# Optimization experiments

Hardware: AMD Instinct MI355X
Metric: run time of the kernel (lower is better)

The kernel has to match this reference:

```python
import jax, jax.numpy as jnp
import numpy as np

B, S, H = 1, 2048, 1024
NH, HD = 16, 64          # num heads, head dim (H = NH*HD)
NT = 1024                # param token num (qkv_slot_num = proj_slot_num)


def pattention(x, key_tokens, value_tokens):
    """Pattention with gelu_l2_norm: x:[...,H] -> [...,out]."""
    attn = jnp.einsum('bsh,th->bst', x, key_tokens)          # scale_factor = 1
    g = jax.nn.gelu(attn, approximate=False)                 # torch F.gelu exact
    norm = jnp.linalg.norm(g, axis=-1, keepdims=True)
    w = g / norm * jnp.sqrt(jnp.asarray(g.shape[-1], g.dtype))
    return jnp.einsum('bst,td->bsd', w, value_tokens)


def setup_inputs() -> dict:
    key = jax.random.key(0)
    ks = jax.random.split(key, 9)
    names = ['q_key', 'q_val', 'k_key', 'k_val', 'v_key', 'v_val', 'proj_key', 'proj_val']
    inp = {'x': jax.random.normal(ks[0], (B, S, H), jnp.float32)}
    for i, n in enumerate(names):
        inp[n] = jax.random.normal(ks[i + 1], (NT, H), jnp.float32) * 0.02
    return inp


def reference(x, q_key, q_val, k_key, k_val, v_key, v_val, proj_key, proj_val):
    # Q/K/V via Pattention (token-parameter attention)
    q = pattention(x, q_key, q_val).reshape(B, S, NH, HD)
    k = pattention(x, k_key, k_val).reshape(B, S, NH, HD)
    v = pattention(x, v_key, v_val).reshape(B, S, NH, HD)
    # causal softmax attention, scale = 1/sqrt(head_dim) (flash default)
    scale = 1.0 / jnp.sqrt(jnp.asarray(HD, q.dtype))
    scores = jnp.einsum('bqhd,bkhd->bhqk', q, k) * scale
    causal = jnp.tril(jnp.ones((S, S), dtype=bool))
    scores = jnp.where(causal, scores, jnp.asarray(-1e30, scores.dtype))
    probs = jax.nn.softmax(scores, axis=-1)
    ctx = jnp.einsum('bhqk,bkhd->bqhd', probs, v).reshape(B, S, H)
    # output projection via Pattention
    return pattention(ctx, proj_key, proj_val)
```

## Files before the change

### kernel.cpp

```cpp
#include <hip/hip_runtime.h>
#include <cstdint>
#include <cstddef>

#define S_LEN 2048
#define H_DIM 1024
#define NTOK  1024
#define NHEAD 16
#define HDIM  64
#define NSPLIT 2

typedef __bf16 bf16;
typedef __bf16 bf16x8 __attribute__((ext_vector_type(8)));
typedef __bf16 bf16x4 __attribute__((ext_vector_type(4)));
typedef __bf16 bf16x2 __attribute__((ext_vector_type(2)));
typedef float  f32x4  __attribute__((ext_vector_type(4)));

#define QSCALE_LOG2E 0.18033688011112042f

static __device__ __forceinline__ f32x4 mfma16(bf16x8 a, bf16x8 b, f32x4 c) {
    return __builtin_amdgcn_mfma_f32_16x16x32_bf16(a, b, c, 0, 0, 0);
}

static __device__ __forceinline__ void async16(const void* gp, void* lp) {
    __builtin_amdgcn_global_load_lds(
        (const __attribute__((address_space(1))) void*)gp,
        (__attribute__((address_space(3))) void*)lp, 16, 0, 0);
}

static __device__ __forceinline__ float fexp2(float x) {
    return __builtin_amdgcn_exp2f(x);
}

#define DRAIN_BARRIER() \
    asm volatile("s_waitcnt vmcnt(0)\n\ts_barrier" ::: "memory")

struct PrepArgs {
    const float* csrc[6];
    bf16* cdst[6];
    const float* tsrc[4];
    bf16* tdst[4];
    float* ssq;
};
__global__ __launch_bounds__(256) void prep_kernel(PrepArgs a) {
    __shared__ float t[64][65];
    if (blockIdx.y < 6) {
        if (blockIdx.y == 0 && blockIdx.x == 0) {
#pragma unroll
            for (int i = 0; i < 24; ++i) a.ssq[threadIdx.x + i * 256] = 0.0f;
        }
        const float* __restrict__ s = a.csrc[blockIdx.y];
        bf16* __restrict__ d = a.cdst[blockIdx.y];
        size_t i = ((size_t)blockIdx.x * 256 + threadIdx.x) * 4;
        f32x4 v = *(const f32x4*)&s[i];
        bf16x4 o;
        o[0] = (bf16)v[0]; o[1] = (bf16)v[1]; o[2] = (bf16)v[2]; o[3] = (bf16)v[3];
        *(bf16x4*)&d[i] = o;
    } else {
        if (blockIdx.x >= 256) return;
        const int z = blockIdx.y - 6;
        const float* __restrict__ in = a.tsrc[z];
        bf16* __restrict__ out = a.tdst[z];
        const int bx = (blockIdx.x & 15) * 64, by = (blockIdx.x >> 4) * 64;
        const int c4 = (threadIdx.x & 15) * 4, r0 = threadIdx.x >> 4;
#pragma unroll
        for (int rr = 0; rr < 64; rr += 16) {
            f32x4 v = *(const f32x4*)&in[(size_t)(by + r0 + rr) * 1024 + bx + c4];
#pragma unroll
            for (int j = 0; j < 4; ++j) t[c4 + j][r0 + rr] = v[j];
        }
        __syncthreads();
        const int l2 = (threadIdx.x & 31) * 2, w8 = threadIdx.x >> 5;
#pragma unroll
        for (int rr = 0; rr < 64; rr += 8) {
            int r = w8 + rr;
            bf16x2 o;
            o[0] = (bf16)t[r][l2];
            o[1] = (bf16)t[r][l2 + 1];
            *(bf16x2*)&out[(size_t)(bx + r) * 1024 + by + l2] = o;
        }
    }
}

template <int MODE, typename OutT>
struct GemmArgs {
    const bf16* A[3];
    const bf16* B[3];
    OutT* C[3];
    float* S[3];
    bf16* Ct[3];
    float emul[3];
};

template <int MODE, typename OutT>
__global__ __launch_bounds__(256, 3) void gemm_bt(GemmArgs<MODE, OutT> args) {
    constexpr int Kd = 1024, Nd = 1024, BK = 64;
    const bf16* __restrict__ A = args.A[blockIdx.z];
    const bf16* __restrict__ B = args.B[blockIdx.z];
    OutT* __restrict__ C = args.C[blockIdx.z];
    float* __restrict__ S = args.S[blockIdx.z];
    bf16* __restrict__ Ct = args.Ct[blockIdx.z];
    const float emul = args.emul[blockIdx.z];

    __shared__ __align__(16) bf16 As[2][128 * BK];
    __shared__ __align__(16) bf16 Bs[2][64 * BK];

    const int tid = threadIdx.x;
    const int w = tid >> 6, lane = tid & 63, quad = lane >> 4, m16 = lane & 15;
    const int wm = (w >> 1) * 64, wn = (w & 1) * 32;
    const int bm = blockIdx.y * 128, bn = blockIdx.x * 64;

    const int srow = lane >> 3;
    const int sseg = ((lane & 7) ^ srow) * 8;

    auto stage = [&](int buf, int k0) {
        const bf16* Ab = A + (size_t)bm * Kd + k0;
#pragma unroll
        for (int c = 0; c < 4; ++c) {
            int chunk = w * 4 + c;
            async16(Ab + (size_t)(chunk * 8 + srow) * Kd + sseg,
                    &As[buf][chunk * 512]);
        }
        const bf16* Bb = B + (size_t)bn * Kd + k0;
#pragma unroll
        for (int c = 0; c < 2; ++c) {
            int chunk = w * 2 + c;
            async16(Bb + (size_t)(chunk * 8 + srow) * Kd + sseg,
                    &Bs[buf][chunk * 512]);
        }
    };

    f32x4 acc[4][2] = {};
    stage(0, 0);

    for (int k0 = 0; k0 < Kd; k0 += BK) {
        const int buf = (k0 >> 6) & 1;
        DRAIN_BARRIER();
        if (k0 + BK < Kd) stage(buf ^ 1, k0 + BK);

        bf16x8 a[2][4], b[2][2];
#pragma unroll
        for (int kc = 0; kc < 2; ++kc) {
#pragma unroll
            for (int i = 0; i < 4; ++i) {
                int row = wm + i * 16 + m16;
                a[kc][i] = *(const bf16x8*)
                    &As[buf][row * 64 + (((kc * 4 + quad) ^ (row & 7)) << 3)];
            }
#pragma unroll
            for (int j = 0; j < 2; ++j) {
                int row = wn + j * 16 + m16;
                b[kc][j] = *(const bf16x8*)
                    &Bs[buf][row * 64 + (((kc * 4 + quad) ^ (row & 7)) << 3)];
            }
        }
#pragma unroll
        for (int kc = 0; kc < 2; ++kc)
#pragma unroll
            for (int i = 0; i < 4; ++i)
#pragma unroll
                for (int j = 0; j < 2; ++j)
                    acc[i][j] = mfma16(a[kc][i], b[kc][j], acc[i][j]);
    }

    if (MODE == 1) {
        float sq[4][4] = {};
#pragma unroll
        for (int i = 0; i < 4; ++i)
#pragma unroll
            for (int j = 0; j < 2; ++j)
#pragma unroll
                for (int r = 0; r < 4; ++r) {
                    int row = bm + wm + i * 16 + quad * 4 + r;
                    int col = bn + wn + j * 16 + m16;
                    float v = acc[i][j][r];
                    v = 0.5f * v * (1.0f + erff(v * 0.70710678118654752f));
                    C[(size_t)row * Nd + col] = (OutT)v;
                    sq[i][r] += v * v;
                }
#pragma unroll
        for (int i = 0; i < 4; ++i)
#pragma unroll
            for (int r = 0; r < 4; ++r) {
                float s2 = sq[i][r];
                s2 += __shfl_xor(s2, 1);
                s2 += __shfl_xor(s2, 2);
                s2 += __shfl_xor(s2, 4);
                s2 += __shfl_xor(s2, 8);
                if (m16 == 0)
                    atomicAdd(&S[bm + wm + i * 16 + quad * 4 + r], s2);
            }
        return;
    }

    float scl[4][4];
#pragma unroll
    for (int i = 0; i < 4; ++i)
#pragma unroll
        for (int r = 0; r < 4; ++r)
            scl[i][r] =
                32.0f * rsqrtf(S[bm + wm + i * 16 + quad * 4 + r]) * emul;

    if (Ct != nullptr) {
#pragma unroll
        for (int i = 0; i < 4; ++i)
#pragma unroll
            for (int j = 0; j < 2; ++j) {
                int k = bm + wm + i * 16 + quad * 4;
                int col = bn + wn + j * 16 + m16;
                bf16x4 o4;
#pragma unroll
                for (int r = 0; r < 4; ++r)
                    o4[r] = (bf16)(acc[i][j][r] * scl[i][r]);
                int kb = k >> 6, c = (k >> 3) & 7, off = k & 7;
                int pos = ((c ^ (col & 7)) << 3) + off;
                *(bf16x4*)&Ct[(size_t)col * 2048 + kb * 64 + pos] = o4;
            }
        return;
    }

#pragma unroll
    for (int i = 0; i < 4; ++i)
#pragma unroll
        for (int j = 0; j < 2; ++j)
#pragma unroll
            for (int r = 0; r < 4; ++r) {
                int row = bm + wm + i * 16 + quad * 4 + r;
                int col = bn + wn + j * 16 + m16;
                C[(size_t)row * Nd + col] = (OutT)(acc[i][j][r] * scl[i][r]);
            }
}

template <int MODE, typename OutT>
__global__ __launch_bounds__(256, 2) void gemm_bt64(GemmArgs<MODE, OutT> args) {
    constexpr int Kd = 1024, Nd = 1024, BK = 64;
    const bf16* __restrict__ A = args.A[blockIdx.z];
    const bf16* __restrict__ B = args.B[blockIdx.z];
    OutT* __restrict__ C = args.C[blockIdx.z];
    float* __restrict__ S = args.S[blockIdx.z];
    const float emul = args.emul[blockIdx.z];

    __shared__ __align__(16) bf16 As[2][64 * 64];
    __shared__ __align__(16) bf16 Bs[2][64 * 64];

    const int tid = threadIdx.x;
    const int w = tid >> 6, lane = tid & 63, quad = lane >> 4, m16 = lane & 15;
    const int wm = (w >> 1) * 32, wn = (w & 1) * 32;
    const int bm = blockIdx.y * 64, bn = blockIdx.x * 64;
    const int trow = tid >> 3, t8 = (tid & 7) * 8;

    auto stage = [&](int buf, int k0) {
#pragma unroll
        for (int c = 0; c < 2; ++c) {
            int row = c * 32 + trow;
            int seg = (((tid & 7) ^ (row & 7)) << 3);
            async16(A + (size_t)(bm + row) * Kd + k0 + seg,
                    &As[buf][row * 64 + t8]);
            async16(B + (size_t)(bn + row) * Kd + k0 + seg,
                    &Bs[buf][row * 64 + t8]);
        }
    };

    f32x4 acc[2][2] = {};
    stage(0, 0);

    for (int k0 = 0; k0 < Kd; k0 += BK) {
        const int buf = (k0 >> 6) & 1;
        DRAIN_BARRIER();
        if (k0 + BK < Kd) stage(buf ^ 1, k0 + BK);

        bf16x8 a[2][2], b[2][2];
#pragma unroll
        for (int kc = 0; kc < 2; ++kc) {
#pragma unroll
            for (int i = 0; i < 2; ++i) {
                int row = wm + i * 16 + m16;
                a[kc][i] = *(const bf16x8*)
                    &As[buf][row * 64 + (((kc * 4 + quad) ^ (row & 7)) << 3)];
            }
#pragma unroll
            for (int j = 0; j < 2; ++j) {
                int row = wn + j * 16 + m16;
                b[kc][j] = *(const bf16x8*)
                    &Bs[buf][row * 64 + (((kc * 4 + quad) ^ (row & 7)) << 3)];
            }
        }
#pragma unroll
        for (int kc = 0; kc < 2; ++kc)
#pragma unroll
            for (int i = 0; i < 2; ++i)
#pragma unroll
                for (int j = 0; j < 2; ++j)
                    acc[i][j] = mfma16(a[kc][i], b[kc][j], acc[i][j]);
    }

    if (MODE == 1) {
        float sq[2][4] = {};
#pragma unroll
        for (int i = 0; i < 2; ++i)
#pragma unroll
            for (int j = 0; j < 2; ++j)
#pragma unroll
                for (int r = 0; r < 4; ++r) {
                    int row = bm + wm + i * 16 + quad * 4 + r;
                    int col = bn + wn + j * 16 + m16;
                    float v = acc[i][j][r];
                    v = 0.5f * v * (1.0f + erff(v * 0.70710678118654752f));
                    C[(size_t)row * Nd + col] = (OutT)v;
                    sq[i][r] += v * v;
                }
#pragma unroll
        for (int i = 0; i < 2; ++i)
#pragma unroll
            for (int r = 0; r < 4; ++r) {
                float s2 = sq[i][r];
                s2 += __shfl_xor(s2, 1);
                s2 += __shfl_xor(s2, 2);
                s2 += __shfl_xor(s2, 4);
                s2 += __shfl_xor(s2, 8);
                if (m16 == 0)
                    atomicAdd(&S[bm + wm + i * 16 + quad * 4 + r], s2);
            }
        return;
    }

    float scl[2][4];
#pragma unroll
    for (int i = 0; i < 2; ++i)
#pragma unroll
        for (int r = 0; r < 4; ++r)
            scl[i][r] =
                32.0f * rsqrtf(S[bm + wm + i * 16 + quad * 4 + r]) * emul;

#pragma unroll
    for (int i = 0; i < 2; ++i)
#pragma unroll
        for (int j = 0; j < 2; ++j)
#pragma unroll
            for (int r = 0; r < 4; ++r) {
                int row = bm + wm + i * 16 + quad * 4 + r;
                int col = bn + wn + j * 16 + m16;
                C[(size_t)row * Nd + col] = (OutT)(acc[i][j][r] * scl[i][r]);
            }
}

struct FlashArgs {
    const bf16* Q;
    const bf16* K;
    const bf16* VtG;
    bf16* op[NSPLIT];
    float* ml;
};

__global__ __launch_bounds__(256, 3) void flash_kernel(FlashArgs fa) {
    const int bid = blockIdx.x;
    const int h = (bid & 7) * 2 + ((bid >> 3) & 1);
    const int s = (bid >> 4) & 1;
    const int qt = 31 - (bid >> 5);
    const int tid = threadIdx.x;
    const int w = tid >> 6, lane = tid & 63, quad = lane >> 4, m16 = lane & 15;
    const int hOff = h * HDIM;

    __shared__ __align__(16) bf16 Ks[2][64 * 64];
    __shared__ __align__(16) bf16 Vs[2][64 * 64];
    __shared__ __align__(16) bf16 Pw[4][16][72];

    const bf16* VtH = fa.VtG + (size_t)hOff * 2048;
    bf16* __restrict__ Opart = fa.op[s];

    const int trow = tid >> 3, tseg8 = (tid & 7) * 8;

    auto stage = [&](int buf, int k0) {
#pragma unroll
        for (int c = 0; c < 2; ++c) {
            int row = c * 32 + trow;
            int seg = (((tid & 7) ^ (row & 7)) << 3);
            async16(fa.K + (size_t)(k0 + row) * H_DIM + hOff + seg,
                    &Ks[buf][row * 64 + tseg8]);
        }
#pragma unroll
        for (int p = 0; p < 2; ++p) {
            int d = trow + p * 32;
            async16(VtH + (size_t)d * 2048 + k0 + tseg8,
                    &Vs[buf][d * 64 + tseg8]);
        }
    };

    const int qRow = qt * 64 + w * 16 + m16;
    bf16x8 bq[2];
    bq[0] = *(const bf16x8*)&fa.Q[(size_t)qRow * H_DIM + hOff + quad * 8];
    bq[1] = *(const bf16x8*)&fa.Q[(size_t)qRow * H_DIM + hOff + 32 + quad * 8];

    f32x4 oacc[4] = {};
    float m_i = -1e30f, l_i = 0.0f;

    const int cnt = (qt >= s) ? ((qt - s) >> 1) + 1 : 0;
    if (cnt > 0) {
        stage(0, s * 64);
        DRAIN_BARRIER();
    }
    for (int i = 0; i < cnt; ++i) {
        const int kt = s + i * NSPLIT;
        const int k0 = kt * 64;
        const int cur = i & 1;
        const bool diag = (kt == qt);
        if (i + 1 < cnt) stage(cur ^ 1, (kt + NSPLIT) * 64);
        f32x4 sacc[4] = {};
        __builtin_amdgcn_s_setprio(1);
#pragma unroll
        for (int ks = 0; ks < 2; ++ks)
#pragma unroll
            for (int j = 0; j < 4; ++j) {
                int row = j * 16 + m16;
                bf16x8 ak = *(const bf16x8*)
                    &Ks[cur][row * 64 + (((ks * 4 + quad) ^ (row & 7)) << 3)];
                sacc[j] = mfma16(ak, bq[ks], sacc[j]);
            }
        __builtin_amdgcn_s_setprio(0);
        if (diag) {
#pragma unroll
            for (int j = 0; j < 4; ++j)
#pragma unroll
                for (int rr = 0; rr < 4; ++rr) {
                    int kcol = k0 + j * 16 + quad * 4 + rr;
                    if (kcol > qRow) sacc[j][rr] = -1e30f;
                }
        }
        float tj[4];
#pragma unroll
        for (int j = 0; j < 4; ++j)
            tj[j] = fmaxf(fmaxf(sacc[j][0], sacc[j][1]),
                          fmaxf(sacc[j][2], sacc[j][3]));
        float mx = fmaxf(fmaxf(tj[0], tj[1]), fmaxf(tj[2], tj[3]));
        mx = fmaxf(mx, __shfl_xor(mx, 16));
        mx = fmaxf(mx, __shfl_xor(mx, 32));
        if (!__all(mx - m_i <= 11.5f)) {
            float mnew = fmaxf(m_i, mx);
            float alpha = fexp2(m_i - mnew);
            l_i *= alpha;
#pragma unroll
            for (int jd = 0; jd < 4; ++jd)
#pragma unroll
                for (int rr = 0; rr < 4; ++rr) oacc[jd][rr] *= alpha;
            m_i = mnew;
        }
        float lsj[4];
#pragma unroll
        for (int j = 0; j < 4; ++j) {
            bf16x4 pk;
            float p0 = fexp2(sacc[j][0] - m_i);
            float p1 = fexp2(sacc[j][1] - m_i);
            float p2 = fexp2(sacc[j][2] - m_i);
            float p3 = fexp2(sacc[j][3] - m_i);
            pk[0] = (bf16)p0; pk[1] = (bf16)p1;
            pk[2] = (bf16)p2; pk[3] = (bf16)p3;
            lsj[j] = (p0 + p1) + (p2 + p3);
            *(bf16x4*)&Pw[w][m16][j * 16 + quad * 4] = pk;
        }
        float ls = (lsj[0] + lsj[1]) + (lsj[2] + lsj[3]);
        ls += __shfl_xor(ls, 16);
        ls += __shfl_xor(ls, 32);
        l_i += ls;
        __builtin_amdgcn_s_setprio(1);
#pragma unroll
        for (int ks = 0; ks < 2; ++ks) {
            bf16x8 bp = *(const bf16x8*)&Pw[w][m16][ks * 32 + quad * 8];
#pragma unroll
            for (int jd = 0; jd < 4; ++jd) {
                int d = jd * 16 + m16;
                bf16x8 av = *(const bf16x8*)
                    &Vs[cur][d * 64 + (((ks * 4 + quad) ^ (d & 7)) << 3)];
                oacc[jd] = mfma16(av, bp, oacc[jd]);
            }
        }
        __builtin_amdgcn_s_setprio(0);
        DRAIN_BARRIER();
    }
#pragma unroll
    for (int jd = 0; jd < 4; ++jd) {
        bf16x4 o4;
#pragma unroll
        for (int rr = 0; rr < 4; ++rr) o4[rr] = (bf16)oacc[jd][rr];
        *(bf16x4*)&Opart[(size_t)qRow * 1024 + hOff + jd * 16 + quad * 4] = o4;
    }
    if (quad == 0) {
        float* p = fa.ml + ((size_t)(s * 2048 + qRow) * 16 + h) * 2;
        p[0] = m_i;
        p[1] = l_i;
    }
}

struct CombArgs {
    const bf16* op[NSPLIT];
    const float* ml;
    bf16* ctx;
    float* ssp;
};
__global__ __launch_bounds__(256) void combine_kernel(CombArgs ca) {
    if (blockIdx.x < 8) ca.ssp[blockIdx.x * 256 + threadIdx.x] = 0.0f;
    const int unit = blockIdx.x * 4 + (threadIdx.x >> 6);
    const int row = unit >> 4, h = unit & 15;
    const int d = threadIdx.x & 63;
    float mv[NSPLIT], lv[NSPLIT], M = -1e30f;
#pragma unroll
    for (int s2 = 0; s2 < NSPLIT; ++s2) {
        const float* p = ca.ml + ((size_t)(s2 * 2048 + row) * 16 + h) * 2;
        mv[s2] = p[0];
        lv[s2] = p[1];
        M = fmaxf(M, mv[s2]);
    }
    float num = 0.0f, den = 0.0f;
#pragma unroll
    for (int s2 = 0; s2 < NSPLIT; ++s2) {
        float e = fexp2(mv[s2] - M);
        den += lv[s2] * e;
        num += e * (float)ca.op[s2][(size_t)row * 1024 + h * 64 + d];
    }
    ca.ctx[(size_t)row * 1024 + h * 64 + d] = (bf16)(num / den);
}

extern "C" void kernel_launch(void* const* d_in, const int* in_sizes, int n_in,
                              void* d_out, int out_size, void* d_ws,
                              size_t ws_size, hipStream_t stream) {
    const float* x = (const float*)d_in[0];
    const float* keysF[4] = {(const float*)d_in[1], (const float*)d_in[3],
                             (const float*)d_in[5], (const float*)d_in[7]};
    const float* valsF[4] = {(const float*)d_in[2], (const float*)d_in[4],
                             (const float*)d_in[6], (const float*)d_in[8]};
    float* out = (float*)d_out;

    char* ws = (char*)d_ws;
    bf16* xb = (bf16*)(ws);
    bf16* g3[3];
    for (int i = 0; i < 3; ++i) g3[i] = (bf16*)(ws + (4ull << 20) + (size_t)i * (4ull << 20));
    bf16* kb16[4], *vT16[4];
    for (int i = 0; i < 4; ++i) {
        kb16[i] = (bf16*)(ws + (16ull << 20) + (size_t)i * (2ull << 20));
        vT16[i] = (bf16*)(ws + (24ull << 20) + (size_t)i * (2ull << 20));
    }
    bf16* qb    = (bf16*)(ws);
    bf16* kbuf  = (bf16*)(ws + (32ull << 20));
    float* mlbuf = (float*)(ws + (20ull << 20));
    bf16* VtG   = (bf16*)(ws + (36ull << 20));
    bf16* ctx   = (bf16*)(ws + (32ull << 20));
    bf16* projg = (bf16*)(ws + (4ull << 20));

    float* SSq = (float*)d_out;
    float* SSp = (float*)(ws + (21ull << 20));

    bf16* opart[NSPLIT];
    for (int i = 0; i < NSPLIT; ++i)
        opart[i] = (bf16*)(ws + (4ull << 20) + (size_t)i * (4ull << 20));

    PrepArgs pa;
    pa.csrc[0] = x;             pa.cdst[0] = xb;
    pa.csrc[1] = x + (1 << 20); pa.cdst[1] = xb + (1 << 20);
    for (int i = 0; i < 4; ++i) { pa.csrc[2 + i] = keysF[i]; pa.cdst[2 + i] = kb16[i]; }
    for (int i = 0; i < 4; ++i) { pa.tsrc[i] = valsF[i]; pa.tdst[i] = vT16[i]; }
    pa.ssq = SSq;
    prep_kernel<<<dim3(1024, 10), 256, 0, stream>>>(pa);

    GemmArgs<1, bf16> g1;
    for (int z = 0; z < 3; ++z) {
        g1.A[z] = xb; g1.B[z] = kb16[z]; g1.C[z] = g3[z];
        g1.S[z] = SSq + z * 2048; g1.Ct[z] = nullptr; g1.emul[z] = 1.0f;
    }
    gemm_bt<1, bf16><<<dim3(16, 16, 3), 256, 0, stream>>>(g1);

    GemmArgs<2, bf16> g2;
    bf16* qkv[3] = {qb, kbuf, qb };
    for (int z = 0; z < 3; ++z) {
        g2.A[z] = g3[z]; g2.B[z] = vT16[z]; g2.C[z] = qkv[z];
        g2.S[z] = SSq + z * 2048;
        g2.Ct[z] = (z == 2) ? VtG : nullptr;
        g2.emul[z] = (z == 0) ? QSCALE_LOG2E : 1.0f;
    }
    gemm_bt<2, bf16><<<dim3(16, 16, 3), 256, 0, stream>>>(g2);

    FlashArgs fla;
    fla.Q = qb; fla.K = kbuf; fla.VtG = VtG; fla.ml = mlbuf;
    for (int i = 0; i < NSPLIT; ++i) fla.op[i] = opart[i];
    flash_kernel<<<dim3(1024), 256, 0, stream>>>(fla);

    CombArgs cba;
    for (int i = 0; i < NSPLIT; ++i) cba.op[i] = opart[i];
    cba.ml = mlbuf; cba.ctx = ctx; cba.ssp = SSp;
    combine_kernel<<<dim3(8192), 256, 0, stream>>>(cba);

    GemmArgs<1, bf16> p1;
    for (int z = 0; z < 3; ++z) {
        p1.A[z] = ctx; p1.B[z] = kb16[3]; p1.C[z] = projg;
        p1.S[z] = SSp; p1.Ct[z] = nullptr; p1.emul[z] = 1.0f;
    }
    gemm_bt64<1, bf16><<<dim3(16, 32, 1), 256, 0, stream>>>(p1);

    GemmArgs<2, float> p2;
    for (int z = 0; z < 3; ++z) {
        p2.A[z] = projg; p2.B[z] = vT16[3]; p2.C[z] = out;
        p2.S[z] = SSp; p2.Ct[z] = nullptr; p2.emul[z] = 1.0f;
    }
    gemm_bt64<2, float><<<dim3(16, 32, 1), 256, 0, stream>>>(p2);
}
```

Before: 208.3 us.

## Replace split-K flash attention and combine kernel with paired q-tile blocks

After: 216.8 us. +4.1%, slower.

```diff
diff --git a/kernel.cpp b/kernel.cpp
--- a/kernel.cpp
+++ b/kernel.cpp
@@ -7,7 +7,6 @@
 #define NTOK  1024
 #define NHEAD 16
 #define HDIM  64
-#define NSPLIT 2
 
 typedef __bf16 bf16;
 typedef __bf16 bf16x8 __attribute__((ext_vector_type(8)));
@@ -347,25 +346,25 @@
     const bf16* Q;
     const bf16* K;
     const bf16* VtG;
-    bf16* op[NSPLIT];
-    float* ml;
+    bf16* ctx;
+    float* ssp;
 };
 
 __global__ __launch_bounds__(256, 3) void flash_kernel(FlashArgs fa) {
     const int bid = blockIdx.x;
     const int h = (bid & 7) * 2 + ((bid >> 3) & 1);
-    const int s = (bid >> 4) & 1;
-    const int qt = 31 - (bid >> 5);
+    const int pr = bid >> 4;
     const int tid = threadIdx.x;
     const int w = tid >> 6, lane = tid & 63, quad = lane >> 4, m16 = lane & 15;
     const int hOff = h * HDIM;
 
+    if (bid < 8) fa.ssp[bid * 256 + tid] = 0.0f;
+
     __shared__ __align__(16) bf16 Ks[2][64 * 64];
     __shared__ __align__(16) bf16 Vs[2][64 * 64];
     __shared__ __align__(16) bf16 Pw[4][16][72];
 
     const bf16* VtH = fa.VtG + (size_t)hOff * 2048;
-    bf16* __restrict__ Opart = fa.op[s];
 
     const int trow = tid >> 3, tseg8 = (tid & 7) * 8;
 
@@ -385,137 +384,105 @@
         }
     };
 
-    const int qRow = qt * 64 + w * 16 + m16;
-    bf16x8 bq[2];
-    bq[0] = *(const bf16x8*)&fa.Q[(size_t)qRow * H_DIM + hOff + quad * 8];
-    bq[1] = *(const bf16x8*)&fa.Q[(size_t)qRow * H_DIM + hOff + 32 + quad * 8];
-
-    f32x4 oacc[4] = {};
-    float m_i = -1e30f, l_i = 0.0f;
-
-    const int cnt = (qt >= s) ? ((qt - s) >> 1) + 1 : 0;
-    if (cnt > 0) {
-        stage(0, s * 64);
+#pragma unroll
+    for (int ti = 0; ti < 2; ++ti) {
+        const int qt = ti ? pr : 31 - pr;
+        const int qRow = qt * 64 + w * 16 + m16;
+        bf16x8 bq[2];
+        bq[0] = *(const bf16x8*)&fa.Q[(size_t)qRow * H_DIM + hOff + quad * 8];
+        bq[1] = *(const bf16x8*)&fa.Q[(size_t)qRow * H_DIM + hOff + 32 + quad * 8];
+
+        f32x4 oacc[4] = {};
+        float m_i = -1e30f, l_i = 0.0f;
+
+        const int cnt = qt + 1;
+        stage(0, 0);
         DRAIN_BARRIER();
-    }
-    for (int i = 0; i < cnt; ++i) {
-        const int kt = s + i * NSPLIT;
-        const int k0 = kt * 64;
-        const int cur = i & 1;
-        const bool diag = (kt == qt);
-        if (i + 1 < cnt) stage(cur ^ 1, (kt + NSPLIT) * 64);
-        f32x4 sacc[4] = {};
-        __builtin_amdgcn_s_setprio(1);
-#pragma unroll
-        for (int ks = 0; ks < 2; ++ks)
+        for (int i = 0; i < cnt; ++i) {
+            const int k0 = i * 64;
+            const int cur = i & 1;
+            const bool diag = (i == qt);
+            if (i + 1 < cnt) stage(cur ^ 1, k0 + 64);
+            f32x4 sacc[4] = {};
+            __builtin_amdgcn_s_setprio(1);
+#pragma unroll
+            for (int ks = 0; ks < 2; ++ks)
+#pragma unroll
+                for (int j = 0; j < 4; ++j) {
+                    int row = j * 16 + m16;
+                    bf16x8 ak = *(const bf16x8*)
+                        &Ks[cur][row * 64 + (((ks * 4 + quad) ^ (row & 7)) << 3)];
+                    sacc[j] = mfma16(ak, bq[ks], sacc[j]);
+                }
+            __builtin_amdgcn_s_setprio(0);
+            if (diag) {
+#pragma unroll
+                for (int j = 0; j < 4; ++j)
+#pragma unroll
+                    for (int rr = 0; rr < 4; ++rr) {
+                        int kcol = k0 + j * 16 + quad * 4 + rr;
+                        if (kcol > qRow) sacc[j][rr] = -1e30f;
+                    }
+            }
+            float tj[4];
+#pragma unroll
+            for (int j = 0; j < 4; ++j)
+                tj[j] = fmaxf(fmaxf(sacc[j][0], sacc[j][1]),
+                              fmaxf(sacc[j][2], sacc[j][3]));
+            float mx = fmaxf(fmaxf(tj[0], tj[1]), fmaxf(tj[2], tj[3]));
+            mx = fmaxf(mx, __shfl_xor(mx, 16));
+            mx = fmaxf(mx, __shfl_xor(mx, 32));
+            if (!__all(mx - m_i <= 11.5f)) {
+                float mnew = fmaxf(m_i, mx);
+                float alpha = fexp2(m_i - mnew);
+                l_i *= alpha;
+#pragma unroll
+                for (int jd = 0; jd < 4; ++jd)
+#pragma unroll
+                    for (int rr = 0; rr < 4; ++rr) oacc[jd][rr] *= alpha;
+                m_i = mnew;
+            }
+            float lsj[4];
 #pragma unroll
             for (int j = 0; j < 4; ++j) {
-                int row = j * 16 + m16;
-                bf16x8 ak = *(const bf16x8*)
-                    &Ks[cur][row * 64 + (((ks * 4 + quad) ^ (row & 7)) << 3)];
-                sacc[j] = mfma16(ak, bq[ks], sacc[j]);
-            }
-        __builtin_amdgcn_s_setprio(0);
-        if (diag) {
-#pragma unroll
-            for (int j = 0; j < 4; ++j)
-#pragma unroll
-                for (int rr = 0; rr < 4; ++rr) {
-                    int kcol = k0 + j * 16 + quad * 4 + rr;
-                    if (kcol > qRow) sacc[j][rr] = -1e30f;
+                bf16x4 pk;
+                float p0 = fexp2(sacc[j][0] - m_i);
+                float p1 = fexp2(sacc[j][1] - m_i);
+                float p2 = fexp2(sacc[j][2] - m_i);
+                float p3 = fexp2(sacc[j][3] - m_i);
+                pk[0] = (bf16)p0; pk[1] = (bf16)p1;
+                pk[2] = (bf16)p2; pk[3] = (bf16)p3;
+                lsj[j] = (p0 + p1) + (p2 + p3);
+                *(bf16x4*)&Pw[w][m16][j * 16 + quad * 4] = pk;
+            }
+            float ls = (lsj[0] + lsj[1]) + (lsj[2] + lsj[3]);
+            ls += __shfl_xor(ls, 16);
+            ls += __shfl_xor(ls, 32);
+            l_i += ls;
+            __builtin_amdgcn_s_setprio(1);
+#pragma unroll
+            for (int ks = 0; ks < 2; ++ks) {
+                bf16x8 bp = *(const bf16x8*)&Pw[w][m16][ks * 32 + quad * 8];
+#pragma unroll
+                for (int jd = 0; jd < 4; ++jd) {
+                    int d = jd * 16 + m16;
+                    bf16x8 av = *(const bf16x8*)
+                        &Vs[cur][d * 64 + (((ks * 4 + quad) ^ (d & 7)) << 3)];
+                    oacc[jd] = mfma16(av, bp, oacc[jd]);
                 }
-        }
-        float tj[4];
-#pragma unroll
-        for (int j = 0; j < 4; ++j)
-            tj[j] = fmaxf(fmaxf(sacc[j][0], sacc[j][1]),
-                          fmaxf(sacc[j][2], sacc[j][3]));
-        float mx = fmaxf(fmaxf(tj[0], tj[1]), fmaxf(tj[2], tj[3]));
-        mx = fmaxf(mx, __shfl_xor(mx, 16));
-        mx = fmaxf(mx, __shfl_xor(mx, 32));
-        if (!__all(mx - m_i <= 11.5f)) {
-            float mnew = fmaxf(m_i, mx);
-            float alpha = fexp2(m_i - mnew);
-            l_i *= alpha;
-#pragma unroll
-            for (int jd = 0; jd < 4; ++jd)
-#pragma unroll
-                for (int rr = 0; rr < 4; ++rr) oacc[jd][rr] *= alpha;
-            m_i = mnew;
-        }
-        float lsj[4];
-#pragma unroll
-        for (int j = 0; j < 4; ++j) {
-            bf16x4 pk;
-            float p0 = fexp2(sacc[j][0] - m_i);
-            float p1 = fexp2(sacc[j][1] - m_i);
-            float p2 = fexp2(sacc[j][2] - m_i);
-            float p3 = fexp2(sacc[j][3] - m_i);
-            pk[0] = (bf16)p0; pk[1] = (bf16)p1;
-            pk[2] = (bf16)p2; pk[3] = (bf16)p3;
-            lsj[j] = (p0 + p1) + (p2 + p3);
-            *(bf16x4*)&Pw[w][m16][j * 16 + quad * 4] = pk;
-        }
-        float ls = (lsj[0] + lsj[1]) + (lsj[2] + lsj[3]);
-        ls += __shfl_xor(ls, 16);
-        ls += __shfl_xor(ls, 32);
-        l_i += ls;
-        __builtin_amdgcn_s_setprio(1);
-#pragma unroll
-        for (int ks = 0; ks < 2; ++ks) {
-            bf16x8 bp = *(const bf16x8*)&Pw[w][m16][ks * 32 + quad * 8];
-#pragma unroll
-            for (int jd = 0; jd < 4; ++jd) {
-                int d = jd * 16 + m16;
-                bf16x8 av = *(const bf16x8*)
-                    &Vs[cur][d * 64 + (((ks * 4 + quad) ^ (d & 7)) << 3)];
-                oacc[jd] = mfma16(av, bp, oacc[jd]);
-            }
-        }
-        __builtin_amdgcn_s_setprio(0);
-        DRAIN_BARRIER();
-    }
-#pragma unroll
-    for (int jd = 0; jd < 4; ++jd) {
-        bf16x4 o4;
-#pragma unroll
-        for (int rr = 0; rr < 4; ++rr) o4[rr] = (bf16)oacc[jd][rr];
-        *(bf16x4*)&Opart[(size_t)qRow * 1024 + hOff + jd * 16 + quad * 4] = o4;
-    }
-    if (quad == 0) {
-        float* p = fa.ml + ((size_t)(s * 2048 + qRow) * 16 + h) * 2;
-        p[0] = m_i;
-        p[1] = l_i;
-    }
-}
-
-struct CombArgs {
-    const bf16* op[NSPLIT];
-    const float* ml;
-    bf16* ctx;
-    float* ssp;
-};
-__global__ __launch_bounds__(256) void combine_kernel(CombArgs ca) {
-    if (blockIdx.x < 8) ca.ssp[blockIdx.x * 256 + threadIdx.x] = 0.0f;
-    const int unit = blockIdx.x * 4 + (threadIdx.x >> 6);
-    const int row = unit >> 4, h = unit & 15;
-    const int d = threadIdx.x & 63;
-    float mv[NSPLIT], lv[NSPLIT], M = -1e30f;
-#pragma unroll
-    for (int s2 = 0; s2 < NSPLIT; ++s2) {
-        const float* p = ca.ml + ((size_t)(s2 * 2048 + row) * 16 + h) * 2;
-        mv[s2] = p[0];
-        lv[s2] = p[1];
-        M = fmaxf(M, mv[s2]);
-    }
-    float num = 0.0f, den = 0.0f;
-#pragma unroll
-    for (int s2 = 0; s2 < NSPLIT; ++s2) {
-        float e = fexp2(mv[s2] - M);
-        den += lv[s2] * e;
-        num += e * (float)ca.op[s2][(size_t)row * 1024 + h * 64 + d];
-    }
-    ca.ctx[(size_t)row * 1024 + h * 64 + d] = (bf16)(num / den);
+            }
+            __builtin_amdgcn_s_setprio(0);
+            DRAIN_BARRIER();
+        }
+        const float inv = 1.0f / l_i;
+#pragma unroll
+        for (int jd = 0; jd < 4; ++jd) {
+            bf16x4 o4;
+#pragma unroll
+            for (int rr = 0; rr < 4; ++rr) o4[rr] = (bf16)(oacc[jd][rr] * inv);
+            *(bf16x4*)&fa.ctx[(size_t)qRow * 1024 + hOff + jd * 16 + quad * 4] = o4;
+        }
+    }
 }
 
 extern "C" void kernel_launch(void* const* d_in, const int* in_sizes, int n_in,
@@ -539,17 +506,12 @@
     }
     bf16* qb    = (bf16*)(ws);
     bf16* kbuf  = (bf16*)(ws + (32ull << 20));
-    float* mlbuf = (float*)(ws + (20ull << 20));
     bf16* VtG   = (bf16*)(ws + (36ull << 20));
-    bf16* ctx   = (bf16*)(ws + (32ull << 20));
-    bf16* projg = (bf16*)(ws + (4ull << 20));
+    bf16* ctx   = (bf16*)(ws + (4ull << 20));
+    bf16* projg = (bf16*)(ws + (8ull << 20));
 
     float* SSq = (float*)d_out;
-    float* SSp = (float*)(ws + (21ull << 20));
-
-    bf16* opart[NSPLIT];
-    for (int i = 0; i < NSPLIT; ++i)
-        opart[i] = (bf16*)(ws + (4ull << 20) + (size_t)i * (4ull << 20));
+    float* SSp = (float*)(ws + (20ull << 20));
 
     PrepArgs pa;
     pa.csrc[0] = x;             pa.cdst[0] = xb;
@@ -577,14 +539,8 @@
     gemm_bt<2, bf16><<<dim3(16, 16, 3), 256, 0, stream>>>(g2);
 
     FlashArgs fla;
-    fla.Q = qb; fla.K = kbuf; fla.VtG = VtG; fla.ml = mlbuf;
-    for (int i = 0; i < NSPLIT; ++i) fla.op[i] = opart[i];
-    flash_kernel<<<dim3(1024), 256, 0, stream>>>(fla);
-
-    CombArgs cba;
-    for (int i = 0; i < NSPLIT; ++i) cba.op[i] = opart[i];
-    cba.ml = mlbuf; cba.ctx = ctx; cba.ssp = SSp;
-    combine_kernel<<<dim3(8192), 256, 0, stream>>>(cba);
+    fla.Q = qb; fla.K = kbuf; fla.VtG = VtG; fla.ctx = ctx; fla.ssp = SSp;
+    flash_kernel<<<dim3(256), 256, 0, stream>>>(fla);
 
     GemmArgs<1, bf16> p1;
     for (int z = 0; z < 3; ++z) {
```
